# Kernel optimization log

Measured on AMD Instinct MI355X. Metric: run time of the kernel, lower is better.

## Reference

```python
import jax, jax.numpy as jnp
import numpy as np

D_MODEL = 512
NUM_HEADS = 8
DK = D_MODEL // NUM_HEADS
SCALE = DK ** -0.5


def setup_inputs() -> dict:
    key = jax.random.key(0)
    ks = jax.random.split(key, 8)
    B, S = 4, 8192
    q = jax.random.normal(ks[0], (B, S, D_MODEL), dtype=jnp.float32)
    k = jax.random.normal(ks[1], (B, S, D_MODEL), dtype=jnp.float32)
    v = jax.random.normal(ks[2], (B, S, D_MODEL), dtype=jnp.float32)
    init = (2.0 / D_MODEL) ** 0.5  # rough kaiming-like scale
    W_q = jax.random.normal(ks[3], (D_MODEL, D_MODEL), dtype=jnp.float32) * init
    W_k = jax.random.normal(ks[4], (D_MODEL, D_MODEL), dtype=jnp.float32) * init
    W_v = jax.random.normal(ks[5], (D_MODEL, D_MODEL), dtype=jnp.float32) * init
    W_o = jax.random.normal(ks[6], (D_MODEL, D_MODEL), dtype=jnp.float32) * init
    b_o = jax.random.normal(ks[7], (D_MODEL,), dtype=jnp.float32) * 0.01
    return {"q": q, "k": k, "v": v, "W_q": W_q, "W_k": W_k, "W_v": W_v, "W_o": W_o, "b_o": b_o}


def reference(q, k, v, W_q, W_k, W_v, W_o, b_o):
    B, S, C = q.shape
    H, dk = NUM_HEADS, DK
    # projections (torch Linear: x @ W.T)
    qh = (q @ W_q.T).reshape(B, S, H, dk).transpose(0, 2, 1, 3)  # [B,H,S,dk]
    kh = (k @ W_k.T).reshape(B, S, H, dk).transpose(0, 2, 1, 3)
    vh = (v @ W_v.T).reshape(B, S, H, dk).transpose(0, 2, 1, 3)
    # linear attention: G = (K^T * scale) @ V  -> [B,H,dk,dk]
    G = jnp.einsum('bhsd,bhse->bhde', kh * SCALE, vh)
    # out = (Q * scale) @ G  -> [B,H,S,dk]
    out = jnp.einsum('bhsd,bhde->bhse', qh * SCALE, G)
    out = out.transpose(0, 2, 1, 3).reshape(B, S, C)
    return out @ W_o.T + b_o
```

## Files before the change

### kernel.cpp

```cpp
#include <hip/hip_runtime.h>
#include <hip/hip_bf16.h>


typedef __attribute__((ext_vector_type(4))) float f32x4;
typedef __attribute__((ext_vector_type(8))) short short8;

#define DEVI __device__ __forceinline__

DEVI unsigned short f2bf(float f) {
  unsigned int u = __builtin_bit_cast(unsigned int, f);
  u += 0x7fffu + ((u >> 16) & 1u);
  return (unsigned short)(u >> 16);
}
DEVI short8 pack8(f32x4 a, f32x4 b) {
  short8 r;
#pragma unroll
  for (int i = 0; i < 4; ++i) { r[i] = (short)f2bf(a[i]); r[i + 4] = (short)f2bf(b[i]); }
  return r;
}

__global__ __launch_bounds__(256, 3) void bigm_kernel(const float* __restrict__ kmat,
                                                      const float* __restrict__ vmat,
                                                      float* __restrict__ Mpart) {
  __shared__ __align__(16) unsigned short Vt[2][128 * 40];
  __shared__ __align__(16) unsigned short Kt[2][128 * 40];
  const int t = threadIdx.x;
  const int bid = blockIdx.x;
  const int xcd = bid & 7, jj = bid >> 3;
  const int p = ((jj >> 4) << 3) | xcd;
  const int tile = jj & 15;
  const int b = p >> 4, split = p & 15;
  const int ti = tile >> 2, tj = tile & 3;
  const int cp0 = ti * 128, ck0 = tj * 128;

  const int lane = t & 63, w = t >> 6;
  const int fr = lane & 15, fg = lane >> 4;
  const int wm = (w >> 1) * 64, wn = (w & 1) * 64;

  const int half = t >> 7;
  const int u = t & 127;
  const int cg = u & 31, sg = u >> 5;
  const float* srcg = (half ? kmat : vmat)
                    + ((size_t)b * 8192 + (size_t)split * 512) * 512
                    + (half ? ck0 : cp0) + cg * 4;
  unsigned short* dstl = (half ? &Kt[0][0] : &Vt[0][0]);
  const int wbase = cg * 4 * 40 + ((sg ^ (cg & 3)) << 3);

  f32x4 r[8];
  auto gload = [&](int sbase) {
    const float* pp = srcg + (size_t)(sbase + sg * 8) * 512;
#pragma unroll
    for (int j = 0; j < 8; ++j) r[j] = *(const f32x4*)(pp + j * 512);
  };
  auto lwrite = [&](int buf) {
    unsigned short* d = dstl + buf * (128 * 40) + wbase;
#pragma unroll
    for (int ci = 0; ci < 4; ++ci) {
      short8 wv;
#pragma unroll
      for (int j = 0; j < 8; ++j) wv[j] = (short)f2bf(r[j][ci]);
      *(short8*)(d + ci * 40) = wv;
    }
  };

  f32x4 acc[4][4] = {};

  gload(0);
  lwrite(0);
  __syncthreads();

  const int key = fr >> 2;
  for (int step = 0; step < 16; ++step) {
    const int cur = step & 1;
    if (step < 15) gload((step + 1) * 32);
    short8 fa[4], fb[4];
#pragma unroll
    for (int i = 0; i < 4; ++i) {
      fa[i] = *(const short8*)&Vt[cur][(wm + i * 16 + fr) * 40 + ((fg ^ key) << 3)];
      fb[i] = *(const short8*)&Kt[cur][(wn + i * 16 + fr) * 40 + ((fg ^ key) << 3)];
    }
#pragma unroll
    for (int i = 0; i < 4; ++i)
#pragma unroll
      for (int j = 0; j < 4; ++j)
        acc[i][j] = __builtin_amdgcn_mfma_f32_16x16x32_bf16(fa[i], fb[j], acc[i][j], 0, 0, 0);
    if (step < 15) lwrite(cur ^ 1);
    __syncthreads();
  }
  float* gp = Mpart + (size_t)p * 262144;
#pragma unroll
  for (int i = 0; i < 4; ++i)
#pragma unroll
    for (int j = 0; j < 4; ++j)
#pragma unroll
      for (int r2 = 0; r2 < 4; ++r2)
        gp[(size_t)(cp0 + wm + i * 16 + fg * 4 + r2) * 512 + ck0 + wn + j * 16 + fr] = acc[i][j][r2];
}

__global__ __launch_bounds__(256) void mred_kernel(const float* __restrict__ Mpart,
                                                   unsigned short* __restrict__ Msum) {
  const int idx = blockIdx.x * 256 + threadIdx.x;
  const int b = idx >> 18;
  const int r = idx & 262143;
  const float* src = Mpart + (size_t)(b * 16) * 262144 + r;
  float s = 0.f;
#pragma unroll
  for (int c = 0; c < 16; ++c) s += src[(size_t)c * 262144];
  Msum[idx] = f2bf(s);
}

__global__ __launch_bounds__(256, 3) void stepa_kernel(const float* __restrict__ Wk,
                                                       const unsigned short* __restrict__ Msum,
                                                       unsigned short* __restrict__ P) {
  __shared__ __align__(16) unsigned short Ab[2][128 * 40];
  __shared__ __align__(16) unsigned short Bb[2][128 * 40];
  const int t = threadIdx.x;
  const int n0 = blockIdx.x * 128;
  const int m0 = blockIdx.y * 128;
  const int b = blockIdx.z;
  const int lane = t & 63, w = t >> 6;
  const int wm = (w >> 1) * 64, wn = (w & 1) * 64;
  const int fr = lane & 15, fg = lane >> 4;
  const int sr = t >> 2;
  const int sk = (t & 3) * 8;

  const float* pAg = Wk + (size_t)(m0 + sr) * 512 + sk;
  const unsigned short* pBg = Msum + (size_t)b * 262144 + (size_t)(n0 + sr) * 512 + sk;

  f32x4 acc[4][4] = {};
  f32x4 a0, a1, a2, a3;
  short8 sb0, sb1;

  a0 = *(const f32x4*)(pAg);         a1 = *(const f32x4*)(pAg + 4);
  a2 = *(const f32x4*)(pAg + 32768); a3 = *(const f32x4*)(pAg + 32772);
  sb0 = *(const short8*)(pBg);
  sb1 = *(const short8*)(pBg + 32768);
  *(short8*)&Ab[0][sr * 40 + sk] = pack8(a0, a1);
  *(short8*)&Ab[0][(sr + 64) * 40 + sk] = pack8(a2, a3);
  *(short8*)&Bb[0][sr * 40 + sk] = sb0;
  *(short8*)&Bb[0][(sr + 64) * 40 + sk] = sb1;
  __syncthreads();

  for (int step = 0; step < 16; ++step) {
    const int cur = step & 1;
    if (step < 15) {
      const int k1 = (step + 1) * 32;
      a0 = *(const f32x4*)(pAg + k1);         a1 = *(const f32x4*)(pAg + k1 + 4);
      a2 = *(const f32x4*)(pAg + k1 + 32768); a3 = *(const f32x4*)(pAg + k1 + 32772);
      sb0 = *(const short8*)(pBg + k1);
      sb1 = *(const short8*)(pBg + k1 + 32768);
    }
    short8 afr[4], bfr[4];
#pragma unroll
    for (int i = 0; i < 4; ++i) {
      afr[i] = *(const short8*)&Ab[cur][(wm + i * 16 + fr) * 40 + fg * 8];
      bfr[i] = *(const short8*)&Bb[cur][(wn + i * 16 + fr) * 40 + fg * 8];
    }
#pragma unroll
    for (int i = 0; i < 4; ++i)
#pragma unroll
      for (int j = 0; j < 4; ++j)
        acc[i][j] = __builtin_amdgcn_mfma_f32_16x16x32_bf16(afr[i], bfr[j], acc[i][j], 0, 0, 0);
    if (step < 15) {
      const int nxt = cur ^ 1;
      *(short8*)&Ab[nxt][sr * 40 + sk] = pack8(a0, a1);
      *(short8*)&Ab[nxt][(sr + 64) * 40 + sk] = pack8(a2, a3);
      *(short8*)&Bb[nxt][sr * 40 + sk] = sb0;
      *(short8*)&Bb[nxt][(sr + 64) * 40 + sk] = sb1;
    }
    __syncthreads();
  }
#pragma unroll
  for (int i = 0; i < 4; ++i)
#pragma unroll
    for (int j = 0; j < 4; ++j)
#pragma unroll
      for (int r = 0; r < 4; ++r) {
        const int row = m0 + wm + i * 16 + fg * 4 + r;
        const int col = n0 + wn + j * 16 + fr;
        P[((size_t)b * 512 + row) * 512 + col] = f2bf(acc[i][j][r]);
      }
}

__global__ __launch_bounds__(64) void stepb_kernel(const unsigned short* __restrict__ P,
                                                   const float* __restrict__ Wv,
                                                   float* __restrict__ Gsum) {
  __shared__ __align__(16) unsigned short Ao[64 * 40];
  __shared__ __align__(16) unsigned short Bo[64 * 40];
  const int t = threadIdx.x;
  const int h = blockIdx.x;
  const int b = blockIdx.y;
  const int fr = t & 15, fg = t >> 4;
  f32x4 acc[4][4] = {};
  for (int step = 0; step < 16; ++step) {
    const int k0 = step * 32;
    const unsigned short* pa = P + ((size_t)b * 512 + h * 64 + t) * 512 + k0;
#pragma unroll
    for (int i = 0; i < 4; ++i) *(short8*)&Ao[t * 40 + i * 8] = *(const short8*)(pa + i * 8);
    const float* pb = Wv + (size_t)(h * 64 + t) * 512 + k0;
#pragma unroll
    for (int i = 0; i < 4; ++i) {
      f32x4 x0 = *(const f32x4*)(pb + i * 8);
      f32x4 x1 = *(const f32x4*)(pb + i * 8 + 4);
      *(short8*)&Bo[t * 40 + i * 8] = pack8(x0, x1);
    }
    __syncthreads();
    short8 afr[4], bfr[4];
#pragma unroll
    for (int i = 0; i < 4; ++i) {
      afr[i] = *(const short8*)&Ao[(i * 16 + fr) * 40 + fg * 8];
      bfr[i] = *(const short8*)&Bo[(i * 16 + fr) * 40 + fg * 8];
    }
#pragma unroll
    for (int i = 0; i < 4; ++i)
#pragma unroll
      for (int j = 0; j < 4; ++j)
        acc[i][j] = __builtin_amdgcn_mfma_f32_16x16x32_bf16(afr[i], bfr[j], acc[i][j], 0, 0, 0);
    __syncthreads();
  }
  float* gout = Gsum + (size_t)(b * 8 + h) * 4096;
#pragma unroll
  for (int i = 0; i < 4; ++i)
#pragma unroll
    for (int j = 0; j < 4; ++j)
#pragma unroll
      for (int r = 0; r < 4; ++r)
        gout[(i * 16 + fg * 4 + r) * 64 + (j * 16 + fr)] = acc[i][j][r] * 0.015625f;
}

__global__ __launch_bounds__(256) void t3_kernel(const float* __restrict__ Wq,
                                                 const float* __restrict__ Gsum,
                                                 unsigned short* __restrict__ T3) {
  __shared__ float Wl[64][64];
  __shared__ float Gl[64][64];
  const int t = threadIdx.x;
  const int c0 = blockIdx.x * 64;
  const int h = blockIdx.y;
  const int b = blockIdx.z;
  const int dd = t >> 2;
  const int c4 = (t & 3) * 16;
  const float* wp = Wq + (size_t)(h * 64 + dd) * 512 + c0 + c4;
  const float* gp = Gsum + (size_t)(b * 8 + h) * 4096 + dd * 64 + c4;
#pragma unroll
  for (int i = 0; i < 4; ++i) {
    *(f32x4*)&Wl[dd][c4 + i * 4] = *(const f32x4*)(wp + i * 4);
    *(f32x4*)&Gl[dd][c4 + i * 4] = *(const f32x4*)(gp + i * 4);
  }
  __syncthreads();
  const int cl0 = (t >> 4) * 4;
  const int e0 = (t & 15) * 4;
  float acc[4][4] = {};
  for (int d = 0; d < 64; ++d) {
    f32x4 wv = *(const f32x4*)&Wl[d][cl0];
    f32x4 gv = *(const f32x4*)&Gl[d][e0];
#pragma unroll
    for (int i = 0; i < 4; ++i)
#pragma unroll
      for (int j = 0; j < 4; ++j)
        acc[i][j] += wv[i] * gv[j];
  }
#pragma unroll
  for (int i = 0; i < 4; ++i)
#pragma unroll
    for (int j = 0; j < 4; ++j)
      T3[((size_t)b * 512 + c0 + cl0 + i) * 512 + h * 64 + e0 + j] = f2bf(acc[i][j]);
}

__global__ __launch_bounds__(64) void wc_kernel(const float* __restrict__ Wo,
                                                const unsigned short* __restrict__ T3,
                                                unsigned short* __restrict__ WcT) {
  __shared__ __align__(16) unsigned short Ao[64 * 48];
  __shared__ __align__(16) unsigned short Bo[64 * 48];
  const int t = threadIdx.x;
  const int n0 = blockIdx.x * 64;
  const int c0 = blockIdx.y * 64;
  const int b = blockIdx.z;
  const int fr = t & 15, fg = t >> 4;
  f32x4 acc[4][4] = {};
  for (int step = 0; step < 16; ++step) {
    const int k0 = step * 32;
    const float* pa = Wo + (size_t)(n0 + t) * 512 + k0;
    unsigned short tmp[32];
#pragma unroll
    for (int i = 0; i < 8; ++i) {
      f32x4 vv = *(const f32x4*)(pa + i * 4);
#pragma unroll
      for (int j = 0; j < 4; ++j) tmp[i * 4 + j] = f2bf(vv[j]);
    }
#pragma unroll
    for (int i = 0; i < 4; ++i) *(short8*)&Ao[t * 48 + i * 8] = *(const short8*)&tmp[i * 8];
    const unsigned short* pb = T3 + ((size_t)b * 512 + c0 + t) * 512 + k0;
#pragma unroll
    for (int i = 0; i < 4; ++i) *(short8*)&Bo[t * 48 + i * 8] = *(const short8*)(pb + i * 8);
    __syncthreads();
    short8 afr[4], bfr[4];
#pragma unroll
    for (int i = 0; i < 4; ++i) {
      afr[i] = *(const short8*)&Ao[(i * 16 + fr) * 48 + fg * 8];
      bfr[i] = *(const short8*)&Bo[(i * 16 + fr) * 48 + fg * 8];
    }
#pragma unroll
    for (int i = 0; i < 4; ++i)
#pragma unroll
      for (int j = 0; j < 4; ++j)
        acc[i][j] = __builtin_amdgcn_mfma_f32_16x16x32_bf16(afr[i], bfr[j], acc[i][j], 0, 0, 0);
    __syncthreads();
  }
#pragma unroll
  for (int i = 0; i < 4; ++i)
#pragma unroll
    for (int j = 0; j < 4; ++j)
#pragma unroll
      for (int r = 0; r < 4; ++r)
        WcT[((size_t)b * 512 + n0 + i * 16 + fg * 4 + r) * 512 + c0 + j * 16 + fr] =
            f2bf(acc[i][j][r]);
}

__global__ __launch_bounds__(256, 4) void out_kernel(const float* __restrict__ q,
                                                     const unsigned short* __restrict__ WcT,
                                                     const float* __restrict__ bo,
                                                     float* __restrict__ Out) {
  __shared__ __align__(16) unsigned short Ab[2][128 * 40];
  __shared__ __align__(16) unsigned short Bb[2][128 * 40];
  const int t = threadIdx.x;
  const int bid = blockIdx.x;
  const int xcd = bid & 7, idx = bid >> 3;
  const int mt = xcd * 32 + (idx >> 2);
  const int nt = idx & 3;
  const int m0 = mt * 128, n0 = nt * 128;
  const unsigned short* Wc = WcT + ((size_t)(m0 >> 13)) * 512 * 512;
  const int lane = t & 63, w = t >> 6;
  const int wm = (w >> 1) * 64, wn = (w & 1) * 64;
  const int fr = lane & 15, fg = lane >> 4;
  const int sr = t >> 2;
  const int sk = (t & 3) * 8;

  const float* pAg = q + (size_t)(m0 + sr) * 512 + sk;
  const unsigned short* pBg = Wc + (size_t)(n0 + sr) * 512 + sk;

  f32x4 acc[4][4] = {};
  f32x4 a0, a1, a2, a3;
  short8 sb0, sb1;

  a0 = *(const f32x4*)(pAg);         a1 = *(const f32x4*)(pAg + 4);
  a2 = *(const f32x4*)(pAg + 32768); a3 = *(const f32x4*)(pAg + 32772);
  sb0 = *(const short8*)(pBg);
  sb1 = *(const short8*)(pBg + 32768);
  *(short8*)&Ab[0][sr * 40 + sk] = pack8(a0, a1);
  *(short8*)&Ab[0][(sr + 64) * 40 + sk] = pack8(a2, a3);
  *(short8*)&Bb[0][sr * 40 + sk] = sb0;
  *(short8*)&Bb[0][(sr + 64) * 40 + sk] = sb1;
  __syncthreads();

  for (int step = 0; step < 16; ++step) {
    const int cur = step & 1;
    if (step < 15) {
      const int k1 = (step + 1) * 32;
      a0 = *(const f32x4*)(pAg + k1);         a1 = *(const f32x4*)(pAg + k1 + 4);
      a2 = *(const f32x4*)(pAg + k1 + 32768); a3 = *(const f32x4*)(pAg + k1 + 32772);
      sb0 = *(const short8*)(pBg + k1);
      sb1 = *(const short8*)(pBg + k1 + 32768);
    }
    short8 afr[4], bfr[4];
#pragma unroll
    for (int i = 0; i < 4; ++i) {
      afr[i] = *(const short8*)&Ab[cur][(wm + i * 16 + fr) * 40 + fg * 8];
      bfr[i] = *(const short8*)&Bb[cur][(wn + i * 16 + fr) * 40 + fg * 8];
    }
#pragma unroll
    for (int i = 0; i < 4; ++i)
#pragma unroll
      for (int j = 0; j < 4; ++j)
        acc[i][j] = __builtin_amdgcn_mfma_f32_16x16x32_bf16(afr[i], bfr[j], acc[i][j], 0, 0, 0);
    if (step < 15) {
      const int nxt = cur ^ 1;
      *(short8*)&Ab[nxt][sr * 40 + sk] = pack8(a0, a1);
      *(short8*)&Ab[nxt][(sr + 64) * 40 + sk] = pack8(a2, a3);
      *(short8*)&Bb[nxt][sr * 40 + sk] = sb0;
      *(short8*)&Bb[nxt][(sr + 64) * 40 + sk] = sb1;
    }
    __syncthreads();
  }
  float bias[4];
#pragma unroll
  for (int j = 0; j < 4; ++j) bias[j] = bo[n0 + wn + j * 16 + fr];
#pragma unroll
  for (int i = 0; i < 4; ++i)
#pragma unroll
    for (int j = 0; j < 4; ++j)
#pragma unroll
      for (int r = 0; r < 4; ++r) {
        const int row = m0 + wm + i * 16 + fg * 4 + r;
        const int col = n0 + wn + j * 16 + fr;
        Out[(size_t)row * 512 + col] = acc[i][j][r] + bias[j];
      }
}

extern "C" void kernel_launch(void* const* d_in, const int* in_sizes, int n_in,
                              void* d_out, int out_size, void* d_ws, size_t ws_size,
                              hipStream_t stream) {
  const float* q  = (const float*)d_in[0];
  const float* k  = (const float*)d_in[1];
  const float* v  = (const float*)d_in[2];
  const float* Wq = (const float*)d_in[3];
  const float* Wk = (const float*)d_in[4];
  const float* Wv = (const float*)d_in[5];
  const float* Wo = (const float*)d_in[6];
  const float* bo = (const float*)d_in[7];
  float* Out = (float*)d_out;

  float* Mpart = (float*)d_out;
  char* ws = (char*)d_ws;
  unsigned short* Msum = (unsigned short*)ws;
  unsigned short* P    = (unsigned short*)(ws + (size_t)2 * 1048576);
  float* Gsum          = (float*)(ws + (size_t)4 * 1048576);
  unsigned short* T3   = (unsigned short*)(ws + (size_t)5 * 1048576);
  unsigned short* WcT  = (unsigned short*)(ws + (size_t)7 * 1048576);

  bigm_kernel<<<1024, 256, 0, stream>>>(k, v, Mpart);
  mred_kernel<<<4096, 256, 0, stream>>>(Mpart, Msum);
  stepa_kernel<<<dim3(4, 4, 4), 256, 0, stream>>>(Wk, Msum, P);
  stepb_kernel<<<dim3(8, 4), 64, 0, stream>>>(P, Wv, Gsum);
  t3_kernel<<<dim3(8, 8, 4), 256, 0, stream>>>(Wq, Gsum, T3);
  wc_kernel<<<dim3(8, 8, 4), 64, 0, stream>>>(Wo, T3, WcT);
  out_kernel<<<1024, 256, 0, stream>>>(q, WcT, bo, Out);
}
```

Measured before the change: 172.7 us.

## Store bf16 partials, vectorize reduction, and load out_kernel fragments directly from global

The k^T·v partial products are now written as bf16 instead of fp32, which halves the partial-buffer traffic, and the reduction kernel reads 8 bf16 values per thread with vector loads. The bigm kernel's launch bound is raised to 4 blocks per CU. The output GEMM drops its LDS double-buffer and has each wave load its MFMA fragments straight from global memory, unrolled by two. The costs are extra rounding in the partial sums and redundant, less coalesced global reads in the output GEMM, since the A and B tiles are no longer shared across waves through LDS.

Result: slower. 220.4 us (+27.7%).

```diff
diff --git a/kernel.cpp b/kernel.cpp
--- a/kernel.cpp
+++ b/kernel.cpp
@@ -12,6 +12,10 @@
   u += 0x7fffu + ((u >> 16) & 1u);
   return (unsigned short)(u >> 16);
 }
+DEVI float bf2f(unsigned short s) {
+  unsigned int u = ((unsigned int)s) << 16;
+  return __builtin_bit_cast(float, u);
+}
 DEVI short8 pack8(f32x4 a, f32x4 b) {
   short8 r;
 #pragma unroll
@@ -19,9 +23,9 @@
   return r;
 }
 
-__global__ __launch_bounds__(256, 3) void bigm_kernel(const float* __restrict__ kmat,
+__global__ __launch_bounds__(256, 4) void bigm_kernel(const float* __restrict__ kmat,
                                                       const float* __restrict__ vmat,
-                                                      float* __restrict__ Mpart) {
+                                                      unsigned short* __restrict__ Mpart) {
   __shared__ __align__(16) unsigned short Vt[2][128 * 40];
   __shared__ __align__(16) unsigned short Kt[2][128 * 40];
   const int t = threadIdx.x;
@@ -87,26 +91,34 @@
     if (step < 15) lwrite(cur ^ 1);
     __syncthreads();
   }
-  float* gp = Mpart + (size_t)p * 262144;
+  unsigned short* gp = Mpart + (size_t)p * 262144;
 #pragma unroll
   for (int i = 0; i < 4; ++i)
 #pragma unroll
     for (int j = 0; j < 4; ++j)
 #pragma unroll
       for (int r2 = 0; r2 < 4; ++r2)
-        gp[(size_t)(cp0 + wm + i * 16 + fg * 4 + r2) * 512 + ck0 + wn + j * 16 + fr] = acc[i][j][r2];
-}
-
-__global__ __launch_bounds__(256) void mred_kernel(const float* __restrict__ Mpart,
+        gp[(size_t)(cp0 + wm + i * 16 + fg * 4 + r2) * 512 + ck0 + wn + j * 16 + fr] =
+            f2bf(acc[i][j][r2]);
+}
+
+__global__ __launch_bounds__(256) void mred_kernel(const unsigned short* __restrict__ Mpart,
                                                    unsigned short* __restrict__ Msum) {
-  const int idx = blockIdx.x * 256 + threadIdx.x;
-  const int b = idx >> 18;
-  const int r = idx & 262143;
-  const float* src = Mpart + (size_t)(b * 16) * 262144 + r;
-  float s = 0.f;
-#pragma unroll
-  for (int c = 0; c < 16; ++c) s += src[(size_t)c * 262144];
-  Msum[idx] = f2bf(s);
+  const int base = (blockIdx.x * 256 + threadIdx.x) * 8;
+  const int b = base >> 18;
+  const int r = base & 262143;
+  const unsigned short* src = Mpart + (size_t)(b * 16) * 262144 + r;
+  float s[8] = {};
+#pragma unroll
+  for (int c = 0; c < 16; ++c) {
+    short8 u = *(const short8*)(src + (size_t)c * 262144);
+#pragma unroll
+    for (int j = 0; j < 8; ++j) s[j] += bf2f((unsigned short)u[j]);
+  }
+  short8 o;
+#pragma unroll
+  for (int j = 0; j < 8; ++j) o[j] = (short)f2bf(s[j]);
+  *(short8*)(Msum + base) = o;
 }
 
 __global__ __launch_bounds__(256, 3) void stepa_kernel(const float* __restrict__ Wk,
@@ -320,8 +332,6 @@
                                                      const unsigned short* __restrict__ WcT,
                                                      const float* __restrict__ bo,
                                                      float* __restrict__ Out) {
-  __shared__ __align__(16) unsigned short Ab[2][128 * 40];
-  __shared__ __align__(16) unsigned short Bb[2][128 * 40];
   const int t = threadIdx.x;
   const int bid = blockIdx.x;
   const int xcd = bid & 7, idx = bid >> 3;
@@ -332,54 +342,26 @@
   const int lane = t & 63, w = t >> 6;
   const int wm = (w >> 1) * 64, wn = (w & 1) * 64;
   const int fr = lane & 15, fg = lane >> 4;
-  const int sr = t >> 2;
-  const int sk = (t & 3) * 8;
-
-  const float* pAg = q + (size_t)(m0 + sr) * 512 + sk;
-  const unsigned short* pBg = Wc + (size_t)(n0 + sr) * 512 + sk;
+
+  const float* pa0 = q + (size_t)(m0 + wm + fr) * 512 + fg * 8;
+  const unsigned short* pb0 = Wc + (size_t)(n0 + wn + fr) * 512 + fg * 8;
 
   f32x4 acc[4][4] = {};
-  f32x4 a0, a1, a2, a3;
-  short8 sb0, sb1;
-
-  a0 = *(const f32x4*)(pAg);         a1 = *(const f32x4*)(pAg + 4);
-  a2 = *(const f32x4*)(pAg + 32768); a3 = *(const f32x4*)(pAg + 32772);
-  sb0 = *(const short8*)(pBg);
-  sb1 = *(const short8*)(pBg + 32768);
-  *(short8*)&Ab[0][sr * 40 + sk] = pack8(a0, a1);
-  *(short8*)&Ab[0][(sr + 64) * 40 + sk] = pack8(a2, a3);
-  *(short8*)&Bb[0][sr * 40 + sk] = sb0;
-  *(short8*)&Bb[0][(sr + 64) * 40 + sk] = sb1;
-  __syncthreads();
-
+#pragma unroll 2
   for (int step = 0; step < 16; ++step) {
-    const int cur = step & 1;
-    if (step < 15) {
-      const int k1 = (step + 1) * 32;
-      a0 = *(const f32x4*)(pAg + k1);         a1 = *(const f32x4*)(pAg + k1 + 4);
-      a2 = *(const f32x4*)(pAg + k1 + 32768); a3 = *(const f32x4*)(pAg + k1 + 32772);
-      sb0 = *(const short8*)(pBg + k1);
-      sb1 = *(const short8*)(pBg + k1 + 32768);
-    }
-    short8 afr[4], bfr[4];
-#pragma unroll
-    for (int i = 0; i < 4; ++i) {
-      afr[i] = *(const short8*)&Ab[cur][(wm + i * 16 + fr) * 40 + fg * 8];
-      bfr[i] = *(const short8*)&Bb[cur][(wn + i * 16 + fr) * 40 + fg * 8];
-    }
-#pragma unroll
-    for (int i = 0; i < 4; ++i)
-#pragma unroll
-      for (int j = 0; j < 4; ++j)
-        acc[i][j] = __builtin_amdgcn_mfma_f32_16x16x32_bf16(afr[i], bfr[j], acc[i][j], 0, 0, 0);
-    if (step < 15) {
-      const int nxt = cur ^ 1;
-      *(short8*)&Ab[nxt][sr * 40 + sk] = pack8(a0, a1);
-      *(short8*)&Ab[nxt][(sr + 64) * 40 + sk] = pack8(a2, a3);
-      *(short8*)&Bb[nxt][sr * 40 + sk] = sb0;
-      *(short8*)&Bb[nxt][(sr + 64) * 40 + sk] = sb1;
-    }
-    __syncthreads();
+    const int k0 = step * 32;
+    short8 fa[4], fb[4];
+#pragma unroll
+    for (int i = 0; i < 4; ++i) {
+      const float* pa = pa0 + (size_t)(i * 16) * 512 + k0;
+      fa[i] = pack8(*(const f32x4*)pa, *(const f32x4*)(pa + 4));
+      fb[i] = *(const short8*)(pb0 + (size_t)(i * 16) * 512 + k0);
+    }
+#pragma unroll
+    for (int i = 0; i < 4; ++i)
+#pragma unroll
+      for (int j = 0; j < 4; ++j)
+        acc[i][j] = __builtin_amdgcn_mfma_f32_16x16x32_bf16(fa[i], fb[j], acc[i][j], 0, 0, 0);
   }
   float bias[4];
 #pragma unroll
@@ -409,7 +391,7 @@
   const float* bo = (const float*)d_in[7];
   float* Out = (float*)d_out;
 
-  float* Mpart = (float*)d_out;
+  unsigned short* Mpart = (unsigned short*)d_out;
   char* ws = (char*)d_ws;
   unsigned short* Msum = (unsigned short*)ws;
   unsigned short* P    = (unsigned short*)(ws + (size_t)2 * 1048576);
@@ -418,7 +400,7 @@
   unsigned short* WcT  = (unsigned short*)(ws + (size_t)7 * 1048576);
 
   bigm_kernel<<<1024, 256, 0, stream>>>(k, v, Mpart);
-  mred_kernel<<<4096, 256, 0, stream>>>(Mpart, Msum);
+  mred_kernel<<<512, 256, 0, stream>>>(Mpart, Msum);
   stepa_kernel<<<dim3(4, 4, 4), 256, 0, stream>>>(Wk, Msum, P);
   stepb_kernel<<<dim3(8, 4), 64, 0, stream>>>(P, Wv, Gsum);
   t3_kernel<<<dim3(8, 8, 4), 256, 0, stream>>>(Wq, Gsum, T3);
```
